# Performance work log

Hardware: AMD Instinct MI355X
Metric: run time of the kernel (lower is better)

## Reference

```python
import jax, jax.numpy as jnp
import numpy as np

EMBED = 512
HEADS = 8
HEAD_DIM = EMBED // HEADS


def setup_inputs() -> dict:
    key = jax.random.key(0)
    ks = jax.random.split(key, 7)
    N, Q, K = 8, 2048, 4096
    s = 1.0 / np.sqrt(EMBED)
    return {
        "x": jax.random.normal(ks[0], (N, Q, EMBED), dtype=jnp.float32),
        "y": jax.random.normal(ks[1], (N, K, EMBED), dtype=jnp.float32),
        "Wq": jax.random.normal(ks[2], (EMBED, EMBED), dtype=jnp.float32) * s,
        "Wk": jax.random.normal(ks[3], (EMBED, EMBED), dtype=jnp.float32) * s,
        "Wv": jax.random.normal(ks[4], (EMBED, EMBED), dtype=jnp.float32) * s,
        "Wo": jax.random.normal(ks[5], (EMBED, EMBED), dtype=jnp.float32) * s,
        "bo": jax.random.normal(ks[6], (EMBED,), dtype=jnp.float32) * 0.01,
    }


def reference(x, y, Wq, Wk, Wv, Wo, bo):
    N, Q, _ = x.shape
    K = y.shape[1]
    # torch Linear: out = in @ W.T
    queries = (x @ Wq.T).reshape(N, Q, HEADS, HEAD_DIM)
    keys = (y @ Wk.T).reshape(N, K, HEADS, HEAD_DIM)
    values = (y @ Wv.T).reshape(N, K, HEADS, HEAD_DIM)
    # NOTE: heads are SUMMED in the score einsum (head-collapsed attention)
    energy = jnp.einsum("nqhd,nkhd->nqk", queries, keys)  # [N,Q,K]
    attention = jax.nn.softmax(energy / jnp.sqrt(jnp.float32(EMBED)), axis=2)
    out = jnp.einsum("nqk,nkhd->nqhd", attention, values).reshape(N, Q, EMBED)
    return x + out @ Wo.T + bo
```

## Files before the change

kernel.cpp:

```cpp
#include <hip/hip_runtime.h>
#include <stdint.h>

typedef unsigned short u16;
typedef short bf16x8 __attribute__((ext_vector_type(8)));
typedef float f32x4 __attribute__((ext_vector_type(4)));
typedef u16 u16x8 __attribute__((ext_vector_type(8)));
typedef u16 u16x4v __attribute__((ext_vector_type(4)));
typedef uint32_t u32x2 __attribute__((ext_vector_type(2)));

#define EMBED 512
#define NBATCH 8
#define QLEN 2048
#define KLEN 4096

__device__ __forceinline__ u16 f2bf(float f) {
  uint32_t u = __builtin_bit_cast(uint32_t, f);
  u += 0x7fffu + ((u >> 16) & 1u);
  return (u16)(u >> 16);
}
__device__ __forceinline__ float bf2f(u16 b) {
  return __builtin_bit_cast(float, (uint32_t)b << 16);
}

__device__ __forceinline__ void gload_lds16(const void* g, void* lds) {
  __builtin_amdgcn_global_load_lds(
      (__attribute__((address_space(1))) void*)(uintptr_t)g,
      (__attribute__((address_space(3))) void*)(uint32_t)(uintptr_t)lds,
      16, 0, 0);
}

__global__ __launch_bounds__(256) void cvt_all_kernel(
    const float* __restrict__ x, const float* __restrict__ y,
    const float* __restrict__ wq, const float* __restrict__ wk,
    const float* __restrict__ wv, const float* __restrict__ wo,
    u16* __restrict__ dst) {
  const int64_t B0 = 2097152;
  const int64_t B1 = B0 + 4194304;
  const int64_t B2 = B1 + 65536;
  const int64_t B3 = B2 + 65536;
  const int64_t B4 = B3 + 65536;
  int64_t i = (int64_t)blockIdx.x * 256 + threadIdx.x;
  const float* src; int64_t off;
  if (i < B0)      { src = x;  off = 0;  }
  else if (i < B1) { src = y;  off = B0; }
  else if (i < B2) { src = wq; off = B1; }
  else if (i < B3) { src = wk; off = B2; }
  else if (i < B4) { src = wv; off = B3; }
  else             { src = wo; off = B4; }
  float4 f = ((const float4*)src)[i - off];
  u16x4v o = { f2bf(f.x), f2bf(f.y), f2bf(f.z), f2bf(f.w) };
  ((u16x4v*)dst)[i] = o;
}

constexpr int EPI_BF16 = 0;
constexpr int EPI_BF16_SCALE = 1;
constexpr int EPI_BF16_TRANS = 2;
constexpr int EPI_F32_RESID = 3;

template <int MODE>
__global__ __launch_bounds__(256, 2) void gemm_bt(
    const u16* __restrict__ A, const u16* __restrict__ B, void* __restrict__ Cv,
    int M, int N, int K,
    int64_t aBatch, int64_t bBatch, int64_t cBatch,
    float scale, const float* __restrict__ xres, const float* __restrict__ bias,
    u16* __restrict__ Vt) {
  __shared__ __align__(16) u16 As[128 * 64];
  __shared__ __align__(16) u16 Bs[128 * 64];

  const int tid = threadIdx.x;
  const int wave = tid >> 6;
  const int lane = tid & 63;
  const int bz = blockIdx.z;
  const int row0 = blockIdx.x * 128;
  const int col0 = blockIdx.y * 128;
  const u16* Ab = A + (int64_t)bz * aBatch;
  const u16* Bb = B + (int64_t)bz * bBatch;

  const int srow = wave * 32 + (lane >> 3);
  const int scol = (lane & 7) * 8;
  const u16* aSrc = Ab + (int64_t)(row0 + srow) * K + scol;
  const u16* bSrc = Bb + (int64_t)(col0 + srow) * K + scol;

  const int wm = (wave >> 1) * 64;
  const int wn = (wave & 1) * 64;
  const int fr = lane & 15;
  const int fq = lane >> 4;

  f32x4 acc[4][4];
#pragma unroll
  for (int mi = 0; mi < 4; ++mi)
#pragma unroll
    for (int ni = 0; ni < 4; ++ni) acc[mi][ni] = 0.0f;

  const int nkt = K >> 6;
  for (int kt = 0; kt < nkt; ++kt) {
    __syncthreads();
    const u16* aS = aSrc + kt * 64;
    const u16* bS = bSrc + kt * 64;
#pragma unroll
    for (int i = 0; i < 4; ++i) {
      gload_lds16(aS + (int64_t)(i * 8) * K, &As[(wave * 32 + i * 8) * 64]);
      gload_lds16(bS + (int64_t)(i * 8) * K, &Bs[(wave * 32 + i * 8) * 64]);
    }
    __syncthreads();
#pragma unroll
    for (int ks = 0; ks < 2; ++ks) {
      bf16x8 af[4], bfr[4];
#pragma unroll
      for (int mi = 0; mi < 4; ++mi)
        af[mi] = *(const bf16x8*)&As[(wm + mi * 16 + fr) * 64 + ks * 32 + fq * 8];
#pragma unroll
      for (int ni = 0; ni < 4; ++ni)
        bfr[ni] = *(const bf16x8*)&Bs[(wn + ni * 16 + fr) * 64 + ks * 32 + fq * 8];
#pragma unroll
      for (int mi = 0; mi < 4; ++mi)
#pragma unroll
        for (int ni = 0; ni < 4; ++ni)
          acc[mi][ni] = __builtin_amdgcn_mfma_f32_16x16x32_bf16(af[mi], bfr[ni],
                                                                acc[mi][ni], 0, 0, 0);
    }
  }

  if constexpr (MODE == EPI_BF16 || MODE == EPI_BF16_SCALE) {
    u16* C = (u16*)Cv + (int64_t)bz * cBatch;
#pragma unroll
    for (int mi = 0; mi < 4; ++mi) {
      const int rowb = row0 + wm + mi * 16 + fq * 4;
#pragma unroll
      for (int ni = 0; ni < 4; ++ni) {
        const int col = col0 + wn + ni * 16 + fr;
#pragma unroll
        for (int r = 0; r < 4; ++r) {
          float v = acc[mi][ni][r];
          if constexpr (MODE == EPI_BF16_SCALE) v *= scale;
          C[(int64_t)(rowb + r) * N + col] = f2bf(v);
        }
      }
    }
  } else if constexpr (MODE == EPI_BF16_TRANS) {
#pragma unroll
    for (int mi = 0; mi < 4; ++mi) {
      const int rowb = row0 + wm + mi * 16 + fq * 4;
      const int nb = rowb >> 12;
      const int kk = rowb & 4095;
#pragma unroll
      for (int ni = 0; ni < 4; ++ni) {
        const int col = col0 + wn + ni * 16 + fr;
        u16x4v o = { f2bf(acc[mi][ni][0]), f2bf(acc[mi][ni][1]),
                     f2bf(acc[mi][ni][2]), f2bf(acc[mi][ni][3]) };
        *(u16x4v*)&Vt[((int64_t)nb * EMBED + col) * KLEN + kk] = o;
      }
    }
  } else {
    float* C = (float*)Cv;
#pragma unroll
    for (int mi = 0; mi < 4; ++mi) {
      const int rowb = row0 + wm + mi * 16 + fq * 4;
#pragma unroll
      for (int ni = 0; ni < 4; ++ni) {
        const int col = col0 + wn + ni * 16 + fr;
        const float bv = bias[col];
#pragma unroll
        for (int r = 0; r < 4; ++r) {
          const int64_t idx = (int64_t)(rowb + r) * N + col;
          C[idx] = acc[mi][ni][r] + xres[idx] + bv;
        }
      }
    }
  }
}

__global__ __launch_bounds__(256, 1) void attn_kernel(
    const u16* __restrict__ Qm, const u16* __restrict__ Km,
    const u16* __restrict__ Vt, u16* __restrict__ O) {
  __shared__ __align__(16) u16 Ks[2][32 * 512];
  __shared__ __align__(16) u16 Vs[2][512 * 32];
  __shared__ __align__(16) u16 Pls[4 * 512];
  __shared__ __align__(16) float Als[64];

  const int tid = threadIdx.x;
  const int w = tid >> 6;
  const int lane = tid & 63;
  const int fr = lane & 15, fq = lane >> 4;
  const int s7 = fr & 7;
  const int frk = fr & 6;
  const int nb = blockIdx.x & 7;
  const int qt = blockIdx.x >> 3;

  bf16x8 q[16];
  {
    const u16* Qb = Qm + ((int64_t)nb * QLEN + qt * 64 + w * 16 + fr) * EMBED + fq * 8;
#pragma unroll
    for (int kc = 0; kc < 16; ++kc) q[kc] = *(const bf16x8*)&Qb[kc * 32];
  }

  f32x4 o[32];
#pragma unroll
  for (int i = 0; i < 32; ++i) o[i] = 0.0f;
  float mrun = -1e30f, lrun = 0.0f;

  const u16* Kb = Km + (int64_t)nb * KLEN * EMBED;
  const u16* Vb = Vt + (int64_t)nb * (int64_t)EMBED * KLEN;

  const int vrow = lane >> 2;
  const int vcl = (lane & 3) ^ ((lane >> 3) & 3);
  const int vswz = ((fr >> 1) & 3);

  {
    const u16* srcK = Kb + (int64_t)(w * 8) * EMBED;
#pragma unroll
    for (int i = 0; i < 8; ++i)
      gload_lds16(srcK + (int64_t)i * EMBED + (lane ^ i) * 8, &Ks[0][(w * 8 + i) * 512]);
#pragma unroll
    for (int i = 0; i < 8; ++i) {
      const int row0 = w * 128 + i * 16;
      gload_lds16(Vb + (int64_t)(row0 + vrow) * KLEN + vcl * 8, &Vs[0][row0 * 32]);
    }
  }
  __syncthreads();

  const int NT = KLEN / 32;
  for (int t = 0; t < NT; ++t) {
    const int cur = t & 1;
    if (t + 1 < NT) {
      const u16* srcK = Kb + ((int64_t)(t + 1) * 32 + w * 8) * EMBED;
#pragma unroll
      for (int i = 0; i < 8; ++i)
        gload_lds16(srcK + (int64_t)i * EMBED + (lane ^ i) * 8,
                    &Ks[cur ^ 1][(w * 8 + i) * 512]);
#pragma unroll
      for (int i = 0; i < 8; ++i) {
        const int row0 = w * 128 + i * 16;
        gload_lds16(Vb + (int64_t)(row0 + vrow) * KLEN + (t + 1) * 32 + vcl * 8,
                    &Vs[cur ^ 1][row0 * 32]);
      }
    }

    const u16* Kc = Ks[cur];
    f32x4 s0 = 0.0f, s1 = 0.0f;
#pragma unroll
    for (int kc = 0; kc < 16; ++kc) {
      bf16x8 k0 = *(const bf16x8*)&Kc[(fr)*512 + (((kc * 4 + fq) ^ s7) * 8)];
      bf16x8 k1 = *(const bf16x8*)&Kc[(16 + fr) * 512 + (((kc * 4 + fq) ^ s7) * 8)];
      s0 = __builtin_amdgcn_mfma_f32_16x16x32_bf16(k0, q[kc], s0, 0, 0, 0);
      s1 = __builtin_amdgcn_mfma_f32_16x16x32_bf16(k1, q[kc], s1, 0, 0, 0);
    }

    const u16* Vc = Vs[cur];
    bf16x8 vb[8];
#pragma unroll
    for (int dt = 0; dt < 8; ++dt)
      vb[dt] = *(const bf16x8*)&Vc[((w * 128 + dt * 16) + fr) * 32 + ((fq ^ vswz) * 8)];

    float mt = fmaxf(fmaxf(fmaxf(s0[0], s0[1]), fmaxf(s0[2], s0[3])),
                     fmaxf(fmaxf(s1[0], s1[1]), fmaxf(s1[2], s1[3])));
    mt = fmaxf(mt, __shfl_xor(mt, 16));
    mt = fmaxf(mt, __shfl_xor(mt, 32));
    float alpha = 1.0f;
    if (!__all(mt <= mrun + 8.0f)) {
      const float mn = fmaxf(mrun, mt);
      alpha = __expf(mrun - mn);
      lrun *= alpha;
      mrun = mn;
    }
    float p0[4], p1[4];
    float rs = 0.0f;
#pragma unroll
    for (int r = 0; r < 4; ++r) {
      p0[r] = __expf(s0[r] - mrun);
      p1[r] = __expf(s1[r] - mrun);
      rs += p0[r] + p1[r];
    }
    rs += __shfl_xor(rs, 16);
    rs += __shfl_xor(rs, 32);
    lrun += rs;

    const uint32_t lo0 = (uint32_t)f2bf(p0[0]) | ((uint32_t)f2bf(p0[1]) << 16);
    const uint32_t lo1 = (uint32_t)f2bf(p0[2]) | ((uint32_t)f2bf(p0[3]) << 16);
    const uint32_t hi0 = (uint32_t)f2bf(p1[0]) | ((uint32_t)f2bf(p1[1]) << 16);
    const uint32_t hi1 = (uint32_t)f2bf(p1[2]) | ((uint32_t)f2bf(p1[3]) << 16);
    {
      u32x2 wlo = {lo0, lo1}, whi = {hi0, hi1};
      *(u32x2*)&Pls[w * 512 + fr * 32 + ((fq ^ frk) * 4)] = wlo;
      *(u32x2*)&Pls[w * 512 + fr * 32 + (((4 + fq) ^ frk) * 4)] = whi;
    }
    if (fq == 0) Als[w * 16 + fr] = alpha;

    asm volatile("s_waitcnt lgkmcnt(0)" ::: "memory");
    __builtin_amdgcn_sched_barrier(0);
    __builtin_amdgcn_s_barrier();
    __builtin_amdgcn_sched_barrier(0);

    f32x4 ra[4];
#pragma unroll
    for (int qg = 0; qg < 4; ++qg) ra[qg] = *(const f32x4*)&Als[qg * 16 + fq * 4];
    int nz = 0;
#pragma unroll
    for (int qg = 0; qg < 4; ++qg)
#pragma unroll
      for (int r = 0; r < 4; ++r) nz |= (ra[qg][r] != 1.0f);
    if (nz) {
#pragma unroll
      for (int qg = 0; qg < 4; ++qg)
#pragma unroll
        for (int dt = 0; dt < 8; ++dt)
#pragma unroll
          for (int r = 0; r < 4; ++r) o[qg * 8 + dt][r] *= ra[qg][r];
    }

    bf16x8 pa[4];
#pragma unroll
    for (int qg = 0; qg < 4; ++qg)
      pa[qg] = *(const bf16x8*)&Pls[qg * 512 + fr * 32 + (((2 * fq) ^ frk) * 4)];

#pragma unroll
    for (int qg = 0; qg < 4; ++qg)
#pragma unroll
      for (int dt = 0; dt < 8; ++dt)
        o[qg * 8 + dt] = __builtin_amdgcn_mfma_f32_16x16x32_bf16(pa[qg], vb[dt],
                                                                 o[qg * 8 + dt], 0, 0, 0);

    __syncthreads();
  }

  if (fq == 0) Als[w * 16 + fr] = lrun;
  __syncthreads();
  f32x4 li[4];
#pragma unroll
  for (int qg = 0; qg < 4; ++qg) {
    f32x4 lv = *(const f32x4*)&Als[qg * 16 + fq * 4];
#pragma unroll
    for (int r = 0; r < 4; ++r) li[qg][r] = 1.0f / lv[r];
  }
  u16* Ob = O + ((int64_t)nb * QLEN + qt * 64) * EMBED + w * 128;
#pragma unroll
  for (int qg = 0; qg < 4; ++qg)
#pragma unroll
    for (int dt = 0; dt < 8; ++dt)
#pragma unroll
      for (int r = 0; r < 4; ++r)
        Ob[(int64_t)(qg * 16 + fq * 4 + r) * EMBED + dt * 16 + fr] =
            f2bf(o[qg * 8 + dt][r] * li[qg][r]);
}

extern "C" void kernel_launch(void* const* d_in, const int* in_sizes, int n_in,
                              void* d_out, int out_size, void* d_ws, size_t ws_size,
                              hipStream_t stream) {
  const float* x  = (const float*)d_in[0];
  const float* y  = (const float*)d_in[1];
  const float* Wq = (const float*)d_in[2];
  const float* Wk = (const float*)d_in[3];
  const float* Wv = (const float*)d_in[4];
  const float* Wo = (const float*)d_in[5];
  const float* bo = (const float*)d_in[6];
  float* out = (float*)d_out;

  const int64_t nx = (int64_t)NBATCH * QLEN * EMBED;
  const int64_t ny = (int64_t)NBATCH * KLEN * EMBED;
  const int64_t nw = (int64_t)EMBED * EMBED;

  u16* w   = (u16*)d_ws;
  u16* xb  = w;
  u16* O   = w; w += nx;
  u16* yb  = w; w += ny;
  u16* Wqb = w; w += nw;
  u16* Wkb = w; w += nw;
  u16* Wvb = w; w += nw;
  u16* Wob = w; w += nw;
  u16* Qm  = w; w += nx;
  u16* Km  = w; w += ny;
  u16* Vt  = w; w += ny;

  cvt_all_kernel<<<25600, 256, 0, stream>>>(x, y, Wq, Wk, Wv, Wo, xb);

  const float scal = 0.04419417382415922f;
  gemm_bt<EPI_BF16_SCALE><<<dim3(128, 4, 1), 256, 0, stream>>>(
      xb, Wqb, Qm, 16384, EMBED, EMBED, 0, 0, 0, scal, nullptr, nullptr, nullptr);
  gemm_bt<EPI_BF16><<<dim3(256, 4, 1), 256, 0, stream>>>(
      yb, Wkb, Km, 32768, EMBED, EMBED, 0, 0, 0, 1.f, nullptr, nullptr, nullptr);
  gemm_bt<EPI_BF16_TRANS><<<dim3(256, 4, 1), 256, 0, stream>>>(
      yb, Wvb, nullptr, 32768, EMBED, EMBED, 0, 0, 0, 1.f, nullptr, nullptr, Vt);

  attn_kernel<<<NBATCH * 32, 256, 0, stream>>>(Qm, Km, Vt, O);

  gemm_bt<EPI_F32_RESID><<<dim3(128, 4, 1), 256, 0, stream>>>(
      O, Wob, out, 16384, EMBED, EMBED, 0, 0, 0, 1.f, x, bo, nullptr);
}
```

Measured before the change: 421.5 us.

## Software-pipeline P·V of previous tile with QK of current tile

Double-buffers the probability and rescale-factor LDS buffers so the P·V MFMAs for tile t-1 run in iteration t, interleaved with the QK MFMAs and softmax of tile t. This removes the mid-iteration barrier between the softmax write and the P·V read, leaving one barrier per tile, and adds an epilogue that finishes the last tile. The cost is more LDS and more live registers (pa, vb, ra held across the QK phase), which may raise register pressure in an already heavy kernel.

```diff
diff --git a/kernel.cpp b/kernel.cpp
--- a/kernel.cpp
+++ b/kernel.cpp
@@ -175,8 +175,8 @@
     const u16* __restrict__ Vt, u16* __restrict__ O) {
   __shared__ __align__(16) u16 Ks[2][32 * 512];
   __shared__ __align__(16) u16 Vs[2][512 * 32];
-  __shared__ __align__(16) u16 Pls[4 * 512];
-  __shared__ __align__(16) float Als[64];
+  __shared__ __align__(16) u16 Pls[2][4 * 512];
+  __shared__ __align__(16) float Als[2][64];
 
   const int tid = threadIdx.x;
   const int w = tid >> 6;
@@ -222,17 +222,36 @@
   const int NT = KLEN / 32;
   for (int t = 0; t < NT; ++t) {
     const int cur = t & 1;
+    const int prv = cur ^ 1;
+
+    bf16x8 pa[4], vb[8];
+    f32x4 ra[4];
+    if (t > 0) {
+#pragma unroll
+      for (int qg = 0; qg < 4; ++qg)
+        pa[qg] = *(const bf16x8*)&Pls[prv][qg * 512 + fr * 32 + (((2 * fq) ^ frk) * 4)];
+#pragma unroll
+      for (int qg = 0; qg < 4; ++qg)
+        ra[qg] = *(const f32x4*)&Als[prv][qg * 16 + fq * 4];
+#pragma unroll
+      for (int dt = 0; dt < 8; ++dt)
+        vb[dt] = *(const bf16x8*)&Vs[prv][((w * 128 + dt * 16) + fr) * 32 +
+                                          ((fq ^ vswz) * 8)];
+      asm volatile("s_waitcnt lgkmcnt(0)" ::: "memory");
+      __builtin_amdgcn_sched_barrier(0);
+    }
+
     if (t + 1 < NT) {
       const u16* srcK = Kb + ((int64_t)(t + 1) * 32 + w * 8) * EMBED;
 #pragma unroll
       for (int i = 0; i < 8; ++i)
         gload_lds16(srcK + (int64_t)i * EMBED + (lane ^ i) * 8,
-                    &Ks[cur ^ 1][(w * 8 + i) * 512]);
+                    &Ks[prv][(w * 8 + i) * 512]);
 #pragma unroll
       for (int i = 0; i < 8; ++i) {
         const int row0 = w * 128 + i * 16;
         gload_lds16(Vb + (int64_t)(row0 + vrow) * KLEN + (t + 1) * 32 + vcl * 8,
-                    &Vs[cur ^ 1][row0 * 32]);
+                    &Vs[prv][row0 * 32]);
       }
     }
 
@@ -246,11 +265,27 @@
       s1 = __builtin_amdgcn_mfma_f32_16x16x32_bf16(k1, q[kc], s1, 0, 0, 0);
     }
 
-    const u16* Vc = Vs[cur];
-    bf16x8 vb[8];
-#pragma unroll
-    for (int dt = 0; dt < 8; ++dt)
-      vb[dt] = *(const bf16x8*)&Vc[((w * 128 + dt * 16) + fr) * 32 + ((fq ^ vswz) * 8)];
+    if (t > 0) {
+      int nz = 0;
+#pragma unroll
+      for (int qg = 0; qg < 4; ++qg)
+#pragma unroll
+        for (int r = 0; r < 4; ++r) nz |= (ra[qg][r] != 1.0f);
+      if (nz) {
+#pragma unroll
+        for (int qg = 0; qg < 4; ++qg)
+#pragma unroll
+          for (int dt = 0; dt < 8; ++dt)
+#pragma unroll
+            for (int r = 0; r < 4; ++r) o[qg * 8 + dt][r] *= ra[qg][r];
+      }
+#pragma unroll
+      for (int qg = 0; qg < 4; ++qg)
+#pragma unroll
+        for (int dt = 0; dt < 8; ++dt)
+          o[qg * 8 + dt] = __builtin_amdgcn_mfma_f32_16x16x32_bf16(
+              pa[qg], vb[dt], o[qg * 8 + dt], 0, 0, 0);
+    }
 
     float mt = fmaxf(fmaxf(fmaxf(s0[0], s0[1]), fmaxf(s0[2], s0[3])),
                      fmaxf(fmaxf(s1[0], s1[1]), fmaxf(s1[2], s1[3])));
@@ -281,19 +316,28 @@
     const uint32_t hi1 = (uint32_t)f2bf(p1[2]) | ((uint32_t)f2bf(p1[3]) << 16);
     {
       u32x2 wlo = {lo0, lo1}, whi = {hi0, hi1};
-      *(u32x2*)&Pls[w * 512 + fr * 32 + ((fq ^ frk) * 4)] = wlo;
-      *(u32x2*)&Pls[w * 512 + fr * 32 + (((4 + fq) ^ frk) * 4)] = whi;
-    }
-    if (fq == 0) Als[w * 16 + fr] = alpha;
-
-    asm volatile("s_waitcnt lgkmcnt(0)" ::: "memory");
-    __builtin_amdgcn_sched_barrier(0);
-    __builtin_amdgcn_s_barrier();
-    __builtin_amdgcn_sched_barrier(0);
-
+      *(u32x2*)&Pls[cur][w * 512 + fr * 32 + ((fq ^ frk) * 4)] = wlo;
+      *(u32x2*)&Pls[cur][w * 512 + fr * 32 + (((4 + fq) ^ frk) * 4)] = whi;
+    }
+    if (fq == 0) Als[cur][w * 16 + fr] = alpha;
+
+    __syncthreads();
+  }
+
+  {
+    const int prv = (NT - 1) & 1;
+    bf16x8 pa[4], vb[8];
     f32x4 ra[4];
 #pragma unroll
-    for (int qg = 0; qg < 4; ++qg) ra[qg] = *(const f32x4*)&Als[qg * 16 + fq * 4];
+    for (int qg = 0; qg < 4; ++qg)
+      pa[qg] = *(const bf16x8*)&Pls[prv][qg * 512 + fr * 32 + (((2 * fq) ^ frk) * 4)];
+#pragma unroll
+    for (int qg = 0; qg < 4; ++qg)
+      ra[qg] = *(const f32x4*)&Als[prv][qg * 16 + fq * 4];
+#pragma unroll
+    for (int dt = 0; dt < 8; ++dt)
+      vb[dt] = *(const bf16x8*)&Vs[prv][((w * 128 + dt * 16) + fr) * 32 +
+                                        ((fq ^ vswz) * 8)];
     int nz = 0;
 #pragma unroll
     for (int qg = 0; qg < 4; ++qg)
@@ -307,28 +351,20 @@
 #pragma unroll
           for (int r = 0; r < 4; ++r) o[qg * 8 + dt][r] *= ra[qg][r];
     }
-
-    bf16x8 pa[4];
 #pragma unroll
     for (int qg = 0; qg < 4; ++qg)
-      pa[qg] = *(const bf16x8*)&Pls[qg * 512 + fr * 32 + (((2 * fq) ^ frk) * 4)];
-
-#pragma unroll
-    for (int qg = 0; qg < 4; ++qg)
 #pragma unroll
       for (int dt = 0; dt < 8; ++dt)
-        o[qg * 8 + dt] = __builtin_amdgcn_mfma_f32_16x16x32_bf16(pa[qg], vb[dt],
-                                                                 o[qg * 8 + dt], 0, 0, 0);
-
-    __syncthreads();
-  }
-
-  if (fq == 0) Als[w * 16 + fr] = lrun;
+        o[qg * 8 + dt] = __builtin_amdgcn_mfma_f32_16x16x32_bf16(
+            pa[qg], vb[dt], o[qg * 8 + dt], 0, 0, 0);
+  }
+
+  if (fq == 0) Als[0][w * 16 + fr] = lrun;
   __syncthreads();
   f32x4 li[4];
 #pragma unroll
   for (int qg = 0; qg < 4; ++qg) {
-    f32x4 lv = *(const f32x4*)&Als[qg * 16 + fq * 4];
+    f32x4 lv = *(const f32x4*)&Als[0][qg * 16 + fq * 4];
 #pragma unroll
     for (int r = 0; r < 4; ++r) li[qg][r] = 1.0f / lv[r];
   }
```

Measured after the change: 461.6 us. 9.5% more time.
